# Kernel optimization log

Measured on AMD Instinct MI355X. Metric: run time of the kernel, lower is better.

The kernel has to match this reference:

```python
import jax, jax.numpy as jnp
import numpy as np

B = 4096
D = 1024
NUM_CLASSES = 100
TEMPERATURE = 0.5
EPS = 1e-12  # matches F.normalize default eps


def setup_inputs() -> dict:
    key = jax.random.key(0)
    k1, k2, k3 = jax.random.split(key, 3)
    emb_i = jax.random.normal(k1, (B, D), dtype=jnp.float32)
    emb_j = jax.random.normal(k2, (B, D), dtype=jnp.float32)
    labels = jax.random.randint(k3, (B,), 0, NUM_CLASSES, dtype=jnp.int32)
    return {"emb_i": emb_i, "emb_j": emb_j, "labels": labels}


def _l2_normalize(x):
    # F.normalize(x, dim=1): x / max(||x||, eps)
    n = jnp.sqrt(jnp.sum(x * x, axis=1, keepdims=True))
    return x / jnp.maximum(n, EPS)


def reference(emb_i, emb_j, labels):
    z_i = _l2_normalize(emb_i)
    z_j = _l2_normalize(emb_j)
    reps = jnp.concatenate([z_i, z_j], axis=0)          # [2B, D]
    # cosine similarity of already-unit vectors == dot product (GEMM instead
    # of the O(N^2 D) broadcasted elementwise form in the torch code)
    sim = jnp.einsum("nd,md->nm", reps, reps)           # [2B, 2B]

    n2 = 2 * B
    neg_mask = 1.0 - jnp.eye(n2, dtype=sim.dtype)       # exclude self-pairs
    label_t = jnp.concatenate([labels, labels], axis=0)  # [2B]
    ws = (label_t[:, None] == label_t[None, :]).astype(sim.dtype) * neg_mask

    e = jnp.exp(sim / TEMPERATURE)                      # [2B, 2B]
    nominator = jnp.sum(ws * e, axis=1)                 # [2B]
    denominator = jnp.sum(neg_mask * e, axis=1)         # [2B]
    loss_partial = -jnp.log(nominator / denominator)
    return jnp.sum(loss_partial) / (2 * B)
```

## Files before the change

### kernel.cpp

```cpp
#include <hip/hip_runtime.h>
#include <hip/hip_bf16.h>
#include <hip/hip_fp8.h>


#define BHALF 4096
#define N2 8192
#define DK 1024
#define DKB 512
#define TILE 128
#define BKB 64
#define NTILE 64
#define NBLK 2080

typedef __attribute__((ext_vector_type(16))) float f32x16;
typedef __attribute__((ext_vector_type(4))) int v4i;
typedef __attribute__((ext_vector_type(8))) int v8i;
typedef unsigned char u8;
typedef unsigned short u16;

#define EXP_SCALE4 0.0028177637517362566f
#define UNIT_SCALE 0x7f7f7f7f

#define WAITVM(n) asm volatile("s_waitcnt vmcnt(" #n ")" ::: "memory")
#define BAR()     asm volatile("s_barrier" ::: "memory")

static __device__ __forceinline__ float fexp2(float x) {
    float r;
    asm("v_exp_f32 %0, %1\n\ts_nop 1" : "=v"(r) : "v"(x));
    return r;
}

static __device__ __forceinline__ unsigned nib4(float x) {
    unsigned s = (__builtin_bit_cast(unsigned, x) >> 31) << 3;
    float a = fminf(fabsf(x), 6.0f);
    unsigned c;
    if (a < 2.0f)      c = (unsigned)lrintf(a * 2.0f);
    else if (a < 4.0f) c = (unsigned)lrintf(a) + 2u;
    else               c = (a < 5.0f) ? 6u : 7u;
    return s | c;
}

__global__ __launch_bounds__(256) void normalize_kernel(
    const float* __restrict__ emb_i, const float* __restrict__ emb_j,
    u16* __restrict__ reps, float* __restrict__ out) {
    int idx = blockIdx.x * 256 + threadIdx.x;
    if (idx == 0) out[0] = 0.0f;
    int r = blockIdx.x * 4 + (threadIdx.x >> 6);
    int lane = threadIdx.x & 63;
    const float* src = (r < BHALF) ? (emb_i + (size_t)r * DK)
                                   : (emb_j + (size_t)(r - BHALF) * DK);
    const float4* srcv = (const float4*)src;
    float4 v[4];
    float s = 0.f;
#pragma unroll
    for (int k = 0; k < 4; ++k) {
        v[k] = srcv[k * 64 + lane];
        s += v[k].x * v[k].x + v[k].y * v[k].y +
             v[k].z * v[k].z + v[k].w * v[k].w;
    }
#pragma unroll
    for (int m = 1; m <= 32; m <<= 1) s += __shfl_xor(s, m, 64);
    float scale = 32.0f / fmaxf(sqrtf(s), 1e-12f);
    u16* dst = reps + (size_t)r * 256;
#pragma unroll
    for (int k = 0; k < 4; ++k) {
        unsigned p = nib4(v[k].x * scale) |
                     (nib4(v[k].y * scale) << 4) |
                     (nib4(v[k].z * scale) << 8) |
                     (nib4(v[k].w * scale) << 12);
        dst[k * 64 + lane] = (u16)p;
    }
}

__global__ __launch_bounds__(256, 4) void gemm_loss_kernel(
    const u8* __restrict__ reps, const int* __restrict__ labels,
    float2* __restrict__ parts) {
    __shared__ __align__(16) u8 A_s[2][TILE * BKB];
    __shared__ __align__(16) u8 B_s[2][TILE * BKB];
    __shared__ float2 red2[2][128];

    int g = blockIdx.x;
    int rem = (g & 7) * 260 + (g >> 3);
    int bi = 0;
    while (rem >= NTILE - bi) { rem -= NTILE - bi; ++bi; }
    int bj = bi + rem;
    int rowBase = bi * TILE;
    int colBase = bj * TILE;

    int tid = threadIdx.x;
    int w = tid >> 6;
    int lane = tid & 63;
    int wm = w >> 1, wn = w & 1;
    int hk = lane >> 5;
    int l31 = lane & 31;

    f32x16 acc[2][2];
#pragma unroll
    for (int i = 0; i < 2; ++i)
#pragma unroll
        for (int j = 0; j < 2; ++j)
#pragma unroll
            for (int r = 0; r < 16; ++r) acc[i][j][r] = 0.0f;

    int srow = lane >> 2;
    int sbg = (lane & 3) ^ ((srow ^ (srow >> 2)) & 3);
    const u8* gA = reps + (size_t)(rowBase + w * 32 + srow) * DKB + sbg * 16;
    const u8* gB = reps + (size_t)(colBase + w * 32 + srow) * DKB + sbg * 16;

    int rswz = (l31 ^ (l31 >> 2)) & 3;
    unsigned aOff[2][2], bOff[2][2];
#pragma unroll
    for (int i = 0; i < 2; ++i) {
#pragma unroll
        for (int ks = 0; ks < 2; ++ks) {
            int ra = (wm * 64 + i * 32 + l31) * BKB;
            aOff[i][ks] = ra + (((ks * 2 + hk) ^ rswz) << 4);
            int rb = (wn * 64 + i * 32 + l31) * BKB;
            bOff[i][ks] = rb + (((ks * 2 + hk) ^ rswz) << 4);
        }
    }

#define STAGE(buf, kt)                                                       \
    {                                                                        \
        _Pragma("unroll")                                                    \
        for (int c = 0; c < 2; ++c) {                                        \
            int chunk = 2 * w + c;                                           \
            __builtin_amdgcn_global_load_lds(                                \
                (const __attribute__((address_space(1))) void*)              \
                    (gA + (size_t)c * 16 * DKB + (kt) * BKB),                \
                (__attribute__((address_space(3))) void*)                    \
                    &A_s[buf][chunk * 1024], 16, 0, 0);                      \
            __builtin_amdgcn_global_load_lds(                                \
                (const __attribute__((address_space(1))) void*)              \
                    (gB + (size_t)c * 16 * DKB + (kt) * BKB),                \
                (__attribute__((address_space(3))) void*)                    \
                    &B_s[buf][chunk * 1024], 16, 0, 0);                      \
        }                                                                    \
    }
#define COMPUTE(buf)                                                         \
    {                                                                        \
        _Pragma("unroll")                                                    \
        for (int ks = 0; ks < 2; ++ks) {                                     \
            v8i aF[2], bF[2];                                                \
            _Pragma("unroll")                                                \
            for (int i = 0; i < 2; ++i) {                                    \
                v4i a4 = *(const v4i*)&A_s[buf][aOff[i][ks]];                \
                aF[i] = __builtin_shufflevector(a4, a4, 0,1,2,3,-1,-1,-1,-1);\
                v4i b4 = *(const v4i*)&B_s[buf][bOff[i][ks]];                \
                bF[i] = __builtin_shufflevector(b4, b4, 0,1,2,3,-1,-1,-1,-1);\
            }                                                                \
            __builtin_amdgcn_s_setprio(1);                                   \
            _Pragma("unroll")                                                \
            for (int i = 0; i < 2; ++i)                                      \
                _Pragma("unroll")                                            \
                for (int j = 0; j < 2; ++j)                                  \
                    acc[i][j] =                                              \
                        __builtin_amdgcn_mfma_scale_f32_32x32x64_f8f6f4(     \
                            aF[i], bF[j], acc[i][j], 4, 4,                   \
                            0, UNIT_SCALE, 0, UNIT_SCALE);                   \
            __builtin_amdgcn_s_setprio(0);                                   \
        }                                                                    \
    }

    STAGE(0, 0)
    STAGE(1, 1)
    for (int kt = 0; kt < 4; kt += 2) {
        WAITVM(4); BAR();
        COMPUTE(0)
        BAR();
        STAGE(0, kt + 2)
        WAITVM(4); BAR();
        COMPUTE(1)
        BAR();
        STAGE(1, kt + 3)
    }
    WAITVM(4); BAR();
    COMPUTE(0)
    BAR();
    STAGE(0, 6)
    WAITVM(4); BAR();
    COMPUTE(1)
    BAR();
    STAGE(1, 7)
    WAITVM(4); BAR();
    COMPUTE(0)
    WAITVM(0); BAR();
    COMPUTE(1)
#undef STAGE
#undef COMPUTE

    bool offd = (bi != bj);
    int lc[2], gcol[2];
#pragma unroll
    for (int j = 0; j < 2; ++j) {
        gcol[j] = colBase + wn * 64 + j * 32 + l31;
        lc[j] = labels[gcol[j] & (BHALF - 1)];
    }
    ((float*)red2)[tid] = 0.0f;
    ((float*)red2)[tid + 256] = 0.0f;
    __syncthreads();

    float colD[2] = {0.f, 0.f}, colN[2] = {0.f, 0.f};
#pragma unroll
    for (int i = 0; i < 2; ++i) {
        float v[32];
#pragma unroll
        for (int reg = 0; reg < 16; ++reg) {
            int rowIn = (reg & 3) + 8 * (reg >> 2) + 4 * hk;
            int grow = rowBase + wm * 64 + i * 32 + rowIn;
            int labr = labels[grow & (BHALF - 1)];
            float rD = 0.f, rN = 0.f;
#pragma unroll
            for (int j = 0; j < 2; ++j) {
                float e = fexp2(acc[i][j][reg] * EXP_SCALE4);
                if (grow == gcol[j]) e = 0.f;
                bool m = (lc[j] == labr);
                rD += e; if (m) rN += e;
                colD[j] += e; if (m) colN[j] += e;
            }
            v[reg] = rD;
            v[16 + reg] = rN;
        }
#pragma unroll
        for (int step = 0; step < 5; ++step) {
            const int m = 16 >> step;
            const int h = 16 >> step;
            bool up = (l31 & m) != 0;
#pragma unroll
            for (int k = 0; k < h; ++k) {
                float sV = up ? v[k] : v[k + h];
                float kV = up ? v[k + h] : v[k];
                v[k] = kV + __shfl_xor(sV, m, 64);
            }
        }
        {
            int reg = l31 & 15;
            int rowOff = wm * 64 + i * 32 +
                         ((reg & 3) + 8 * (reg >> 2) + 4 * hk);
            float* cell = (l31 & 16) ? &red2[0][rowOff].x
                                     : &red2[0][rowOff].y;
            atomicAdd(cell, v[0]);
        }
    }
    if (offd) {
#pragma unroll
        for (int j = 0; j < 2; ++j) {
            float cd = colD[j] + __shfl_xor(colD[j], 32, 64);
            float cn = colN[j] + __shfl_xor(colN[j], 32, 64);
            if (hk == 0) {
                int colOff = wn * 64 + j * 32 + l31;
                atomicAdd(&red2[1][colOff].x, cn);
                atomicAdd(&red2[1][colOff].y, cd);
            }
        }
    }
    __syncthreads();
    if (tid < 128) {
        parts[(size_t)bj * N2 + rowBase + tid] = red2[0][tid];
    } else if (offd) {
        parts[(size_t)bi * N2 + colBase + tid - 128] = red2[1][tid - 128];
    }
}

__global__ __launch_bounds__(256) void finalize_kernel(
    const float2* __restrict__ parts, float* __restrict__ out) {
    int row = blockIdx.x * 256 + threadIdx.x;
    int t = threadIdx.x;
    float n = 0.f, d = 0.f;
#pragma unroll 8
    for (int s = 0; s < NTILE; ++s) {
        float2 p = parts[(size_t)s * N2 + row];
        n += p.x;
        d += p.y;
    }
    float sv = logf(d) - logf(n);
#pragma unroll
    for (int m = 1; m <= 32; m <<= 1) sv += __shfl_xor(sv, m, 64);
    __shared__ float red[4];
    if ((t & 63) == 0) red[t >> 6] = sv;
    __syncthreads();
    if (t == 0)
        atomicAdd(out, (red[0] + red[1] + red[2] + red[3]) / (float)N2);
}

extern "C" void kernel_launch(void* const* d_in, const int* in_sizes, int n_in,
                              void* d_out, int out_size, void* d_ws, size_t ws_size,
                              hipStream_t stream) {
    const float* emb_i = (const float*)d_in[0];
    const float* emb_j = (const float*)d_in[1];
    const int* labels  = (const int*)d_in[2];
    float* out = (float*)d_out;

    char* ws = (char*)d_ws;
    u8* reps     = (u8*)ws;
    float2* parts = (float2*)(ws + (size_t)N2 * DKB);

    normalize_kernel<<<2048, 256, 0, stream>>>(emb_i, emb_j, (u16*)reps, out);
    gemm_loss_kernel<<<NBLK, 256, 0, stream>>>(reps, labels, parts);
    finalize_kernel<<<(N2 + 255) / 256, 256, 0, stream>>>(parts, out);
}
```

Measured before the change: 124.2 us.

## Switch GEMM K-loop to triple-buffered LDS pipeline with one barrier per stage

Grows the shared-memory staging buffers from two to three and rewrites the unrolled K loop so each step issues the next global-to-LDS stage before computing the current one. This needs only one barrier per step, where before there were two. The red2 zeroing moves to kernel start, which removes a __syncthreads before the epilogue. In exchange, LDS use per block rises and the launch bound drops from 4 to 3 blocks per CU, which may lower occupancy.

```diff
diff --git a/kernel.cpp b/kernel.cpp
--- a/kernel.cpp
+++ b/kernel.cpp
@@ -72,11 +72,11 @@
     }
 }
 
-__global__ __launch_bounds__(256, 4) void gemm_loss_kernel(
+__global__ __launch_bounds__(256, 3) void gemm_loss_kernel(
     const u8* __restrict__ reps, const int* __restrict__ labels,
     float2* __restrict__ parts) {
-    __shared__ __align__(16) u8 A_s[2][TILE * BKB];
-    __shared__ __align__(16) u8 B_s[2][TILE * BKB];
+    __shared__ __align__(16) u8 A_s[3][TILE * BKB];
+    __shared__ __align__(16) u8 B_s[3][TILE * BKB];
     __shared__ float2 red2[2][128];
 
     int g = blockIdx.x;
@@ -93,6 +93,9 @@
     int wm = w >> 1, wn = w & 1;
     int hk = lane >> 5;
     int l31 = lane & 31;
+
+    ((float*)red2)[tid] = 0.0f;
+    ((float*)red2)[tid + 256] = 0.0f;
 
     f32x16 acc[2][2];
 #pragma unroll
@@ -164,28 +167,14 @@
 
     STAGE(0, 0)
     STAGE(1, 1)
-    for (int kt = 0; kt < 4; kt += 2) {
-        WAITVM(4); BAR();
-        COMPUTE(0)
-        BAR();
-        STAGE(0, kt + 2)
-        WAITVM(4); BAR();
-        COMPUTE(1)
-        BAR();
-        STAGE(1, kt + 3)
-    }
-    WAITVM(4); BAR();
-    COMPUTE(0)
-    BAR();
-    STAGE(0, 6)
-    WAITVM(4); BAR();
-    COMPUTE(1)
-    BAR();
-    STAGE(1, 7)
-    WAITVM(4); BAR();
-    COMPUTE(0)
-    WAITVM(0); BAR();
-    COMPUTE(1)
+    WAITVM(4); BAR(); STAGE(2, 2) COMPUTE(0)
+    WAITVM(4); BAR(); STAGE(0, 3) COMPUTE(1)
+    WAITVM(4); BAR(); STAGE(1, 4) COMPUTE(2)
+    WAITVM(4); BAR(); STAGE(2, 5) COMPUTE(0)
+    WAITVM(4); BAR(); STAGE(0, 6) COMPUTE(1)
+    WAITVM(4); BAR(); STAGE(1, 7) COMPUTE(2)
+    WAITVM(4); BAR();             COMPUTE(0)
+    WAITVM(0); BAR();             COMPUTE(1)
 #undef STAGE
 #undef COMPUTE
 
@@ -196,9 +185,6 @@
         gcol[j] = colBase + wn * 64 + j * 32 + l31;
         lc[j] = labels[gcol[j] & (BHALF - 1)];
     }
-    ((float*)red2)[tid] = 0.0f;
-    ((float*)red2)[tid + 256] = 0.0f;
-    __syncthreads();
 
     float colD[2] = {0.f, 0.f}, colN[2] = {0.f, 0.f};
 #pragma unroll
```

New measurement: 124.2 us. Within noise of the previous version (+0.0%).

## Fuse finalize into GEMM via global atomics and last-block reduction

Applied to the files above, without the earlier changes.

Row and column partial sums now go straight into a global nom/den array with atomics, replacing the per-tile partial buffer and the shared-memory staging. The last block, found with an atomic counter, computes the log-ratio sum and writes the loss, so the separate finalize kernel launch is gone. This saves a launch and the partial-buffer traffic, but adds heavy global atomic contention, roughly 64 atomics per row address across blocks. The final reduction also now runs serially in a single block.

```diff
diff --git a/kernel.cpp b/kernel.cpp
--- a/kernel.cpp
+++ b/kernel.cpp
@@ -42,9 +42,11 @@
 
 __global__ __launch_bounds__(256) void normalize_kernel(
     const float* __restrict__ emb_i, const float* __restrict__ emb_j,
-    u16* __restrict__ reps, float* __restrict__ out) {
+    u16* __restrict__ reps, float* __restrict__ nomden,
+    unsigned* __restrict__ counter, float* __restrict__ out) {
     int idx = blockIdx.x * 256 + threadIdx.x;
-    if (idx == 0) out[0] = 0.0f;
+    if (idx < 2 * N2) nomden[idx] = 0.0f;
+    if (idx == 0) { out[0] = 0.0f; counter[0] = 0u; }
     int r = blockIdx.x * 4 + (threadIdx.x >> 6);
     int lane = threadIdx.x & 63;
     const float* src = (r < BHALF) ? (emb_i + (size_t)r * DK)
@@ -74,10 +76,10 @@
 
 __global__ __launch_bounds__(256, 4) void gemm_loss_kernel(
     const u8* __restrict__ reps, const int* __restrict__ labels,
-    float2* __restrict__ parts) {
+    float2* __restrict__ nomden, unsigned* __restrict__ counter,
+    float* __restrict__ out) {
     __shared__ __align__(16) u8 A_s[2][TILE * BKB];
     __shared__ __align__(16) u8 B_s[2][TILE * BKB];
-    __shared__ float2 red2[2][128];
 
     int g = blockIdx.x;
     int rem = (g & 7) * 260 + (g >> 3);
@@ -196,9 +198,6 @@
         gcol[j] = colBase + wn * 64 + j * 32 + l31;
         lc[j] = labels[gcol[j] & (BHALF - 1)];
     }
-    ((float*)red2)[tid] = 0.0f;
-    ((float*)red2)[tid + 256] = 0.0f;
-    __syncthreads();
 
     float colD[2] = {0.f, 0.f}, colN[2] = {0.f, 0.f};
 #pragma unroll
@@ -235,10 +234,10 @@
         }
         {
             int reg = l31 & 15;
-            int rowOff = wm * 64 + i * 32 +
-                         ((reg & 3) + 8 * (reg >> 2) + 4 * hk);
-            float* cell = (l31 & 16) ? &red2[0][rowOff].x
-                                     : &red2[0][rowOff].y;
+            int grow = rowBase + wm * 64 + i * 32 +
+                       ((reg & 3) + 8 * (reg >> 2) + 4 * hk);
+            float* cell = (l31 & 16) ? &nomden[grow].x
+                                     : &nomden[grow].y;
             atomicAdd(cell, v[0]);
         }
     }
@@ -248,39 +247,37 @@
             float cd = colD[j] + __shfl_xor(colD[j], 32, 64);
             float cn = colN[j] + __shfl_xor(colN[j], 32, 64);
             if (hk == 0) {
-                int colOff = wn * 64 + j * 32 + l31;
-                atomicAdd(&red2[1][colOff].x, cn);
-                atomicAdd(&red2[1][colOff].y, cd);
+                atomicAdd(&nomden[gcol[j]].x, cn);
+                atomicAdd(&nomden[gcol[j]].y, cd);
             }
         }
     }
+
     __syncthreads();
-    if (tid < 128) {
-        parts[(size_t)bj * N2 + rowBase + tid] = red2[0][tid];
-    } else if (offd) {
-        parts[(size_t)bi * N2 + colBase + tid - 128] = red2[1][tid - 128];
-    }
-}
-
-__global__ __launch_bounds__(256) void finalize_kernel(
-    const float2* __restrict__ parts, float* __restrict__ out) {
-    int row = blockIdx.x * 256 + threadIdx.x;
-    int t = threadIdx.x;
-    float n = 0.f, d = 0.f;
-#pragma unroll 8
-    for (int s = 0; s < NTILE; ++s) {
-        float2 p = parts[(size_t)s * N2 + row];
-        n += p.x;
-        d += p.y;
-    }
-    float sv = logf(d) - logf(n);
-#pragma unroll
-    for (int m = 1; m <= 32; m <<= 1) sv += __shfl_xor(sv, m, 64);
-    __shared__ float red[4];
-    if ((t & 63) == 0) red[t >> 6] = sv;
+    __shared__ int lastFlag;
+    if (tid == 0) {
+        unsigned prev = __hip_atomic_fetch_add(
+            counter, 1u, __ATOMIC_ACQ_REL, __HIP_MEMORY_SCOPE_AGENT);
+        lastFlag = (prev == NBLK - 1);
+    }
     __syncthreads();
-    if (t == 0)
-        atomicAdd(out, (red[0] + red[1] + red[2] + red[3]) / (float)N2);
+    if (lastFlag) {
+        float s = 0.f;
+        for (int r = tid; r < N2; r += 256) {
+            unsigned long long pv = __hip_atomic_load(
+                (const unsigned long long*)&nomden[r],
+                __ATOMIC_RELAXED, __HIP_MEMORY_SCOPE_AGENT);
+            float2 p = __builtin_bit_cast(float2, pv);
+            s += __logf(p.y) - __logf(p.x);
+        }
+#pragma unroll
+        for (int m = 1; m <= 32; m <<= 1) s += __shfl_xor(s, m, 64);
+        __shared__ float red[4];
+        if ((tid & 63) == 0) red[tid >> 6] = s;
+        __syncthreads();
+        if (tid == 0)
+            out[0] = (red[0] + red[1] + red[2] + red[3]) / (float)N2;
+    }
 }
 
 extern "C" void kernel_launch(void* const* d_in, const int* in_sizes, int n_in,
@@ -292,10 +289,12 @@
     float* out = (float*)d_out;
 
     char* ws = (char*)d_ws;
-    u8* reps     = (u8*)ws;
-    float2* parts = (float2*)(ws + (size_t)N2 * DKB);
-
-    normalize_kernel<<<2048, 256, 0, stream>>>(emb_i, emb_j, (u16*)reps, out);
-    gemm_loss_kernel<<<NBLK, 256, 0, stream>>>(reps, labels, parts);
-    finalize_kernel<<<(N2 + 255) / 256, 256, 0, stream>>>(parts, out);
-}
+    u8* reps        = (u8*)ws;
+    float2* nomden  = (float2*)(ws + (size_t)N2 * DKB);
+    unsigned* counter = (unsigned*)(ws + (size_t)N2 * DKB + N2 * sizeof(float2));
+
+    normalize_kernel<<<2048, 256, 0, stream>>>(emb_i, emb_j, (u16*)reps,
+                                               (float*)nomden, counter, out);
+    gemm_loss_kernel<<<NBLK, 256, 0, stream>>>(reps, labels, nomden,
+                                               counter, out);
+}
```

New measurement: 154.1 us. 1.24x slower.
